# Performance work log

Hardware: AMD Instinct MI355X
Metric: run time of the kernel (lower is better)

Reference implementation:

```python
import jax, jax.numpy as jnp
import numpy as np

EPS = 1e-6      # VN nonlinearity eps
BN_EPS = 1e-5   # torch BatchNorm default eps


def setup_inputs() -> dict:
    key = jax.random.key(0)
    k1, k2, k3 = jax.random.split(key, 3)
    B, Cin, N = 8, 64, 2048
    Cout = 64
    x = jax.random.normal(k1, (B, Cin, 3, N), dtype=jnp.float32)
    # nn.Linear(in, out, bias=False) weights: [out, in], kaiming-uniform-ish scale
    s = 1.0 / np.sqrt(Cin)
    W_feat = jax.random.uniform(k2, (Cout, Cin), jnp.float32, -s, s)
    W_dir = jax.random.uniform(k3, (Cout, Cin), jnp.float32, -s, s)
    gamma = jnp.ones((Cout,), jnp.float32)
    beta = jnp.zeros((Cout,), jnp.float32)
    return {"x": x, "W_feat": W_feat, "W_dir": W_dir, "gamma": gamma, "beta": beta, "k": 10}


def _knn_idx(xf, kk):
    # xf: [B, D, N]; returns indices of kk nearest neighbors (incl. self), [B, N, kk]
    xx = jnp.sum(xf * xf, axis=1)                       # [B, N]
    inner = jnp.einsum('bdn,bdm->bnm', xf, xf)          # [B, N, N]
    pdist = 2.0 * inner - xx[:, :, None] - xx[:, None, :]  # = -||xi-xj||^2
    _, idx = jax.lax.top_k(pdist, kk)                   # largest = nearest
    return idx


def reference(x, W_feat, W_dir, gamma, beta, k):
    B, Cin, _, N = x.shape
    K = k + 1
    xf = x.reshape(B, Cin * 3, N)                       # [B, 3*Cin, N]
    idx = _knn_idx(xf, K)                               # [B, N, K]

    # gather neighbor features: [B, N, K, 3*Cin]
    xT = jnp.transpose(xf, (0, 2, 1))                   # [B, N, 3*Cin]
    feat = jax.vmap(lambda xt, id_: xt[id_])(xT, idx)   # [B, N, K, 3*Cin]
    feat = feat.reshape(B, N, K, Cin, 3)
    feat = jnp.transpose(feat, (0, 3, 4, 1, 2))         # [B, Cin, 3, N, K]

    # VN linear
    p = jnp.einsum('oc,bcdnk->bodnk', W_feat, feat)     # [B, Cout, 3, N, K]

    # VNBatchNorm (training-mode batch stats, biased var) on vector norms
    norm = jnp.sqrt(jnp.sum(p * p, axis=2))             # [B, Cout, N, K]
    mean = jnp.mean(norm, axis=(0, 2, 3))
    var = jnp.var(norm, axis=(0, 2, 3))
    norm_bn = (norm - mean[None, :, None, None]) * jax.lax.rsqrt(var + BN_EPS)[None, :, None, None]
    norm_bn = norm_bn * gamma[None, :, None, None] + beta[None, :, None, None]
    p = p / norm[:, :, None] * norm_bn[:, :, None]

    # direction + conditional vector nonlinearity
    d = jnp.einsum('oc,bcdnk->bodnk', W_dir, feat)      # [B, Cout, 3, N, K]
    dot = jnp.sum(p * d, axis=2, keepdims=True)         # [B, Cout, 1, N, K]
    d_sq = jnp.sum(d * d, axis=2, keepdims=True)
    x_out = jnp.where(dot >= 0, p, p - dot / (d_sq + EPS) * d)

    return jnp.mean(x_out, axis=-1)                     # [B, Cout, 3, N]
```

## Files before the change

kernel.cpp:

```cpp
#include <hip/hip_runtime.h>
#include <stdint.h>

#define B_   8
#define D_   192
#define N_   2048
#define KNb  11

using u32 = uint32_t;
using u16 = unsigned short;
typedef _Float16 f16;
struct alignas(8) h4 { f16 x, y, z, w; };

typedef __attribute__((ext_vector_type(8)))  short short8;
typedef __attribute__((ext_vector_type(16))) float f32x16;

__device__ __forceinline__ u16 f2bf(float f){
  union{float f; u32 i;} x; x.f = f;
  u32 r = (x.i + 0x7fffu + ((x.i >> 16) & 1u)) >> 16;
  return (u16)r;
}
__device__ __forceinline__ u32 umax32(u32 a, u32 b){ return a > b ? a : b; }
__device__ __forceinline__ u32 umin32(u32 a, u32 b){ return a < b ? a : b; }
__device__ __forceinline__ u32 med3_u32(u32 a, u32 b, u32 c){
  u32 d;
  asm("v_med3_u32 %0, %1, %2, %3" : "=v"(d) : "v"(a), "v"(b), "v"(c));
  return d;
}

__device__ __forceinline__ void sel16(const u32* __restrict__ ctp, u32* key){
  #pragma unroll
  for (int q = 0; q < 4; ++q){
    uint4 kv = *(const uint4*)(ctp + 4*q);
    u32 ks[4] = {kv.x, kv.y, kv.z, kv.w};
    #pragma unroll
    for (int j = 0; j < 4; ++j){
      u32 kk = ks[j];
      #pragma unroll
      for (int s = 0; s < 9; ++s) key[s] = med3_u32(kk, key[s], key[s+1]);
      key[9] = umax32(kk, key[9]);
    }
  }
}

__global__ __launch_bounds__(256) void split_kernel(const float* __restrict__ x,
                                                    short* __restrict__ Xs,
                                                    float* __restrict__ xT,
                                                    double* __restrict__ xxd){
  __shared__ float A[D_ * 32];
  const int b = blockIdx.y, tile = blockIdx.x, m0 = tile * 32, t = threadIdx.x;
  const size_t xb = (size_t)b * D_ * N_;
  #pragma unroll
  for (int q = 0; q < 24; ++q){
    int p = t + 256*q;
    int d = p >> 5, i = p & 31;
    A[d*32 + i] = x[xb + (size_t)d*N_ + m0 + i];
  }
  __syncthreads();

  {
    const int l = t & 63, wv = t >> 6;
    const int lh = l >> 5, l31 = l & 31;
    #pragma unroll
    for (int j = 0; j < 3; ++j){
      int c = j*4 + wv;
      int dbase = c*16 + lh*8;
      union{ u16 s[8]; int4 v; } u;
      #pragma unroll
      for (int q = 0; q < 8; ++q) u.s[q] = f2bf(A[(dbase + q)*32 + l31]);
      size_t P = ((size_t)b*64 + tile)*12 + c;
      *(int4*)(Xs + P*512 + l*8) = u.v;
    }
  }
  {
    const int m = t & 31, seg = t >> 5;
    float* trow = xT + ((size_t)b*N_ + m0 + m) * 192 + seg*24;
    #pragma unroll
    for (int j = 0; j < 6; ++j){
      float4 v = { A[(seg*24 + 4*j + 0)*32 + m], A[(seg*24 + 4*j + 1)*32 + m],
                   A[(seg*24 + 4*j + 2)*32 + m], A[(seg*24 + 4*j + 3)*32 + m] };
      *(float4*)(trow + 4*j) = v;
    }
  }
  if (t < 32){
    double s = 0.0;
    #pragma unroll 4
    for (int d = 0; d < D_; ++d){ double v = (double)A[d*32 + t]; s = fma(v, v, s); }
    xxd[b*N_ + m0 + t] = s;
  }
}

#define KLA   0
#define KLCT0 12288
#define KLCT1 45568
#define KLSZ  78848
__global__ __launch_bounds__(512, 4) void knn_kernel(const short* __restrict__ Xs,
                                                     const double* __restrict__ xxd,
                                                     u16* __restrict__ cand){
  __shared__ __align__(16) char smem[KLSZ];

  const int b = blockIdx.x, n0 = blockIdx.y * 32;
  const int t = threadIdx.x, lane = t & 63, w = t >> 6;
  const int l31 = lane & 31, lh = lane >> 5;
  const int mcol = w*32 + l31;

  {
    const short* Ap = Xs + (((size_t)b*64 + (n0 >> 5)) * 12) * 512;
    int4 v = *(const int4*)(Ap + (size_t)t*8);
    *(int4*)(smem + KLA + t*16) = v;
    if (t < 256){
      int p = t + 512;
      int4 v2 = *(const int4*)(Ap + (size_t)p*8);
      *(int4*)(smem + KLA + p*16) = v2;
    }
  }
  float xxn[16];
  #pragma unroll
  for (int reg = 0; reg < 16; ++reg){
    int r = (reg & 3) + 8*(reg >> 2) + 4*lh;
    xxn[reg] = (float)xxd[b*N_ + n0 + r];
  }
  __syncthreads();

  u32 key[10];
  #pragma unroll
  for (int j = 0; j < 10; ++j) key[j] = 0u;

  for (int st = 0; st < 8; ++st){
    const int m0 = st * 256;
    const short* Bp = Xs + (((size_t)b*64 + st*8 + w) * 12) * 512 + lane*8;
    short8 pg[12];
    #pragma unroll
    for (int j = 0; j < 12; ++j) pg[j] = *(const short8*)(Bp + j*512);
    float xxs = (float)xxd[b*N_ + m0 + mcol];

    if (st > 0){
      const u32* ctp = (const u32*)(smem + ((st & 1) ? KLCT0 : KLCT1))
                       + (t & 31)*260 + (t >> 5)*16;
      sel16(ctp, key);
    }

    f32x16 acc = (f32x16)0.0f;
    #pragma unroll
    for (int kc = 0; kc < 6; ++kc){
      short8 a0 = *(const short8*)(smem + KLA + (kc*2+0)*1024 + lane*16);
      short8 a1 = *(const short8*)(smem + KLA + (kc*2+1)*1024 + lane*16);
      acc = __builtin_amdgcn_mfma_f32_32x32x16_bf16(a0, pg[kc*2+0], acc, 0, 0, 0);
      acc = __builtin_amdgcn_mfma_f32_32x32x16_bf16(a1, pg[kc*2+1], acc, 0, 0, 0);
    }

    {
      u32* ctw = (u32*)(smem + ((st & 1) ? KLCT1 : KLCT0));
      const u32 midx = (u32)(m0 + mcol);
      #pragma unroll
      for (int reg = 0; reg < 16; ++reg){
        float v = fmaf(2.f, acc[reg], -(xxs + xxn[reg]));
        u32 bb = __float_as_uint(v);
        u32 kk = ((bb ^ (u32)(((int)bb >> 31) | 0x80000000)) & 0xFFFFF800u) | midx;
        int r = (reg & 3) + 8*(reg >> 2) + 4*lh;
        ctw[r*260 + mcol] = kk;
      }
    }
    __syncthreads();
  }
  {
    const u32* ctp = (const u32*)(smem + KLCT1) + (t & 31)*260 + (t >> 5)*16;
    sel16(ctp, key);
  }

  u32* MVK = (u32*)(smem + KLCT0);
  {
    const int r = t & 31, sub = t >> 5;
    #pragma unroll
    for (int j = 0; j < 10; ++j) MVK[(sub*32 + r)*10 + j] = key[j];
  }
  __syncthreads();
  if (t < 32){
    int head[16];
    #pragma unroll
    for (int q = 0; q < 16; ++q) head[q] = 9;
    const size_t ob = ((size_t)b*N_ + n0 + t) * 16;
    for (int s = 0; s < 16; ++s){
      u32 best = 0u; int bq = 0;
      #pragma unroll
      for (int q = 0; q < 16; ++q){
        int hh = head[q];
        u32 v = (hh >= 0) ? MVK[(q*32 + t)*10 + hh] : 0u;
        if (v > best){ best = v; bq = q; }
      }
      cand[ob + s] = (u16)(best & 2047u);
      #pragma unroll
      for (int q = 0; q < 16; ++q) head[q] -= (q == bq) ? 1 : 0;
    }
  }
}

__global__ __launch_bounds__(256, 3) void refine_kernel(const float* __restrict__ xT,
                                                        const u16* __restrict__ cand,
                                                        const double* __restrict__ xxd,
                                                        int* __restrict__ idxout,
                                                        int* __restrict__ cnt){
  const int wv = threadIdx.x >> 6, ln = threadIdx.x & 63;
  const int b = blockIdx.x & 7;
  const int n = (blockIdx.x >> 3) * 4 + wv;
  const int g = b * N_ + n;
  const int c = ln >> 2, part = ln & 3;
  const int m = (int)cand[(size_t)g*16 + c] & 2047;
  const float4* pn = (const float4*)(xT + ((size_t)b*N_ + n)*192 + part*48);
  const float4* pm = (const float4*)(xT + ((size_t)b*N_ + m)*192 + part*48);
  float4 an[12], am[12];
  #pragma unroll
  for (int j = 0; j < 12; ++j) an[j] = pn[j];
  #pragma unroll
  for (int j = 0; j < 12; ++j) am[j] = pm[j];
  double s0 = 0.0, s1 = 0.0, s2 = 0.0, s3 = 0.0;
  #pragma unroll
  for (int j = 0; j < 12; j += 4){
    s0 = fma((double)an[j+0].x, (double)am[j+0].x, s0);
    s0 = fma((double)an[j+0].y, (double)am[j+0].y, s0);
    s0 = fma((double)an[j+0].z, (double)am[j+0].z, s0);
    s0 = fma((double)an[j+0].w, (double)am[j+0].w, s0);
    s1 = fma((double)an[j+1].x, (double)am[j+1].x, s1);
    s1 = fma((double)an[j+1].y, (double)am[j+1].y, s1);
    s1 = fma((double)an[j+1].z, (double)am[j+1].z, s1);
    s1 = fma((double)an[j+1].w, (double)am[j+1].w, s1);
    s2 = fma((double)an[j+2].x, (double)am[j+2].x, s2);
    s2 = fma((double)an[j+2].y, (double)am[j+2].y, s2);
    s2 = fma((double)an[j+2].z, (double)am[j+2].z, s2);
    s2 = fma((double)an[j+2].w, (double)am[j+2].w, s2);
    s3 = fma((double)an[j+3].x, (double)am[j+3].x, s3);
    s3 = fma((double)an[j+3].y, (double)am[j+3].y, s3);
    s3 = fma((double)an[j+3].z, (double)am[j+3].z, s3);
    s3 = fma((double)an[j+3].w, (double)am[j+3].w, s3);
  }
  double s = (s0 + s1) + (s2 + s3);
  s += __shfl_down(s, 2, 64);
  s += __shfl_down(s, 1, 64);
  double v = 2.0*s - xxd[b*N_ + n] - xxd[b*N_ + m];
  int rank = 0;
  #pragma unroll
  for (int q = 0; q < 16; ++q){
    double vq = __shfl(v, q*4, 64);
    int    mq = __shfl(m, q*4, 64);
    bool beat = (vq > v) || ((vq == v) && (mq < m));
    rank += beat ? 1 : 0;
  }
  if (part == 0 && rank < KNb){
    idxout[(size_t)g*KNb + rank] = m;
    atomicAdd(&cnt[b*N_ + m], 1);
  }
}

__global__ __launch_bounds__(256) void project_kernel(const float* __restrict__ xT,
                                                      const float* __restrict__ Wf,
                                                      const float* __restrict__ Wd,
                                                      h4* __restrict__ P0h,
                                                      h4* __restrict__ D0h){
  __shared__ float A[16 * 192];
  const int b = blockIdx.x, m0 = blockIdx.y * 16, t = threadIdx.x;
  const int l = t & 63, wv = t >> 6;
  const int half = l >> 5;
  const int c = (wv & 1)*32 + (l & 31);
  const int mg = wv >> 1;

  float wfh[32], wdh[32];
  #pragma unroll
  for (int q = 0; q < 8; ++q){
    float4 uf = *(const float4*)(Wf + c*64 + half*32 + q*4);
    wfh[q*4+0]=uf.x; wfh[q*4+1]=uf.y; wfh[q*4+2]=uf.z; wfh[q*4+3]=uf.w;
    float4 ud = *(const float4*)(Wd + c*64 + half*32 + q*4);
    wdh[q*4+0]=ud.x; wdh[q*4+1]=ud.y; wdh[q*4+2]=ud.z; wdh[q*4+3]=ud.w;
  }
  {
    const float4* src = (const float4*)(xT + ((size_t)b*N_ + m0)*192);
    float4* dst = (float4*)A;
    #pragma unroll
    for (int j = 0; j < 3; ++j) dst[t + 256*j] = src[t + 256*j];
  }
  __syncthreads();

  for (int i = 0; i < 8; ++i){
    int m = mg*8 + i;
    const float4* row = (const float4*)(A + m*192 + half*96);
    float p[3] = {0.f,0.f,0.f}, qv[3] = {0.f,0.f,0.f};
    #pragma unroll
    for (int v4 = 0; v4 < 24; ++v4){
      float4 f = row[v4];
      const int e = v4*4;
      p [(e+0)%3] = fmaf(wfh[(e+0)/3], f.x, p [(e+0)%3]);
      qv[(e+0)%3] = fmaf(wdh[(e+0)/3], f.x, qv[(e+0)%3]);
      p [(e+1)%3] = fmaf(wfh[(e+1)/3], f.y, p [(e+1)%3]);
      qv[(e+1)%3] = fmaf(wdh[(e+1)/3], f.y, qv[(e+1)%3]);
      p [(e+2)%3] = fmaf(wfh[(e+2)/3], f.z, p [(e+2)%3]);
      qv[(e+2)%3] = fmaf(wdh[(e+2)/3], f.z, qv[(e+2)%3]);
      p [(e+3)%3] = fmaf(wfh[(e+3)/3], f.w, p [(e+3)%3]);
      qv[(e+3)%3] = fmaf(wdh[(e+3)/3], f.w, qv[(e+3)%3]);
    }
    float o0 = __shfl_xor(p[0], 32, 64), o1 = __shfl_xor(p[1], 32, 64);
    float o2 = __shfl_xor(p[2], 32, 64);
    float u0 = __shfl_xor(qv[0], 32, 64), u1 = __shfl_xor(qv[1], 32, 64);
    float u2 = __shfl_xor(qv[2], 32, 64);
    if (half == 0){
      float t0 = p[0] + o0, t1 = p[1] + o1, t2 = p[2] + o2;
      float r0 = qv[0] + u0, r1 = qv[1] + u1, r2 = qv[2] + u2;
      float nrm = sqrtf(t0*t0 + t1*t1 + t2*t2);
      float dsq = r0*r0 + r1*r1 + r2*r2;
      size_t base = ((size_t)b*N_ + m0 + m)*64 + c;
      h4 vp; vp.x = (f16)t0; vp.y = (f16)t1; vp.z = (f16)t2; vp.w = (f16)nrm;
      h4 vd; vd.x = (f16)r0; vd.y = (f16)r1; vd.z = (f16)r2; vd.w = (f16)dsq;
      P0h[base] = vp;
      D0h[base] = vd;
    }
  }
}

__global__ __launch_bounds__(256) void stats_kernel(const h4* __restrict__ P0h,
                                                    const int* __restrict__ cnt,
                                                    float* __restrict__ gs){
  const int b = blockIdx.x >> 6;
  const int chunk = blockIdx.x & 63;
  const int w = threadIdx.x >> 6, c = threadIdx.x & 63;
  float s = 0.f, s2 = 0.f;
  const int mbase = chunk*32 + w*8;
  for (int i = 0; i < 8; ++i){
    int m = mbase + i;
    float wt = (float)cnt[b*N_ + m];
    float nv = (float)P0h[((size_t)b*N_ + m)*64 + c].w;
    s  = fmaf(wt, nv, s);
    s2 = fmaf(wt*nv, nv, s2);
  }
  __shared__ float red[8][64];
  red[w][c] = s; red[4+w][c] = s2;
  __syncthreads();
  if (w == 0) atomicAdd(&gs[c],    red[0][c]+red[1][c]+red[2][c]+red[3][c]);
  if (w == 1) atomicAdd(&gs[64+c], red[4][c]+red[5][c]+red[6][c]+red[7][c]);
}

__global__ __launch_bounds__(512) void out_kernel(const h4* __restrict__ P0h, const h4* __restrict__ D0h,
                                                  const int* __restrict__ idxin, const float* __restrict__ gs,
                                                  const float* __restrict__ gamma, const float* __restrict__ beta,
                                                  float* __restrict__ outp){
  __shared__ float res[16 * 193];
  const int b  = blockIdx.x;
  const int n0 = blockIdx.y * 16;
  const int t = threadIdx.x, w = t >> 6, c = t & 63;
  const float Ninv = 1.f / (float)(B_*N_*KNb);
  float mean = gs[c] * Ninv;
  float var  = gs[64+c] * Ninv - mean*mean;
  float istd = rsqrtf(var + 1e-5f);
  float sa = istd * gamma[c];
  float be = beta[c];
  const float kinv = 1.f/11.f;
  for (int i = 0; i < 2; ++i){
    int row = w*2 + i;
    int n = n0 + row;
    const int* ip = idxin + ((size_t)b*N_ + n)*KNb;
    float a0=0, a1=0, a2=0;
    #pragma unroll
    for (int k = 0; k < KNb; ++k){
      int m = ip[k] & 2047;
      size_t base = ((size_t)b*N_ + m)*64 + c;
      h4 P  = P0h[base];
      h4 Dv = D0h[base];
      float pw = (float)P.w;
      float nb = (pw - mean)*sa + be;
      float sc = nb / pw;
      float p0 = (float)P.x*sc, p1 = (float)P.y*sc, p2 = (float)P.z*sc;
      float d0 = (float)Dv.x, d1 = (float)Dv.y, d2 = (float)Dv.z;
      float dot = p0*d0 + p1*d1 + p2*d2;
      float f = (dot >= 0.f) ? 0.f : dot / ((float)Dv.w + 1e-6f);
      a0 += p0 - f*d0; a1 += p1 - f*d1; a2 += p2 - f*d2;
    }
    res[row*193 + 3*c + 0] = a0*kinv;
    res[row*193 + 3*c + 1] = a1*kinv;
    res[row*193 + 3*c + 2] = a2*kinv;
  }
  __syncthreads();
  {
    int p = t;
    #pragma unroll
    for (int j = 0; j < 2; ++j){
      if (p < 768){
        int cdim = p >> 2, nq = p & 3;
        float4 v = { res[(nq*4 + 0)*193 + cdim], res[(nq*4 + 1)*193 + cdim],
                     res[(nq*4 + 2)*193 + cdim], res[(nq*4 + 3)*193 + cdim] };
        *(float4*)(outp + ((size_t)b*192 + cdim)*N_ + n0 + nq*4) = v;
      }
      p += 512;
    }
  }
}

extern "C" void kernel_launch(void* const* d_in, const int* in_sizes, int n_in,
                              void* d_out, int out_size, void* d_ws, size_t ws_size,
                              hipStream_t stream){
  const float* x     = (const float*)d_in[0];
  const float* Wf    = (const float*)d_in[1];
  const float* Wd    = (const float*)d_in[2];
  const float* gamma = (const float*)d_in[3];
  const float* beta  = (const float*)d_in[4];
  float* outp = (float*)d_out;

  char* ws = (char*)d_ws;
  int*    idx  = (int*)   (ws);
  int*    cnt  = (int*)   (ws + 720896);
  float*  gs   = (float*) (ws + 786432);
  h4*     P0h  = (h4*)    (ws + 1048576);
  h4*     D0h  = (h4*)    (ws + 9437184);
  short*  Xs   = (short*) (ws + 1048576);
  double* xxd  = (double*)(ws + 13631488);
  u16*    cand = (u16*)   (ws + 13762560);
  float*  xT   = (float*) (ws + 17825792);

  hipMemsetAsync(cnt, 0, 66048, stream);
  split_kernel  <<<dim3(64, 8),  256, 0, stream>>>(x, Xs, xT, xxd);
  knn_kernel    <<<dim3(8, 64),  512, 0, stream>>>(Xs, xxd, cand);
  refine_kernel <<<4096,         256, 0, stream>>>(xT, cand, xxd, idx, cnt);
  project_kernel<<<dim3(8, 128), 256, 0, stream>>>(xT, Wf, Wd, P0h, D0h);
  stats_kernel  <<<512,          256, 0, stream>>>(P0h, cnt, gs);
  out_kernel    <<<dim3(8, 128), 512, 0, stream>>>(P0h, D0h, idx, gs, gamma, beta, outp);
}
```

Measured before the change: 233.0 us.

## Skip idle top-k inserts and merge per-row candidates with wave shuffles

The top-k insertion network now runs only when some lane in the wave has a key larger than its current minimum. The 16 threads that own a query row are made contiguous (row = t>>4), so the final 16-way merge runs as a shuffle-based max reduction across 16 lanes. This replaces the shared-memory dump and the serial merge done by 32 threads. It removes a barrier and the single-warp tail, at the cost of a ballot branch inside the selection loop and a changed LDS access pattern for the candidate reads.

```diff
diff --git a/kernel.cpp b/kernel.cpp
--- a/kernel.cpp
+++ b/kernel.cpp
@@ -35,9 +35,11 @@
     #pragma unroll
     for (int j = 0; j < 4; ++j){
       u32 kk = ks[j];
-      #pragma unroll
-      for (int s = 0; s < 9; ++s) key[s] = med3_u32(kk, key[s], key[s+1]);
-      key[9] = umax32(kk, key[9]);
+      if (__any(kk > key[0])){
+        #pragma unroll
+        for (int s = 0; s < 9; ++s) key[s] = med3_u32(kk, key[s], key[s+1]);
+        key[9] = umax32(kk, key[9]);
+      }
     }
   }
 }
@@ -102,6 +104,7 @@
   const int t = threadIdx.x, lane = t & 63, w = t >> 6;
   const int l31 = lane & 31, lh = lane >> 5;
   const int mcol = w*32 + l31;
+  const int selr = t >> 4, selg = t & 15;
 
   {
     const short* Ap = Xs + (((size_t)b*64 + (n0 >> 5)) * 12) * 512;
@@ -135,7 +138,7 @@
 
     if (st > 0){
       const u32* ctp = (const u32*)(smem + ((st & 1) ? KLCT0 : KLCT1))
-                       + (t & 31)*260 + (t >> 5)*16;
+                       + selr*260 + selg*16;
       sel16(ctp, key);
     }
 
@@ -163,34 +166,25 @@
     __syncthreads();
   }
   {
-    const u32* ctp = (const u32*)(smem + KLCT1) + (t & 31)*260 + (t >> 5)*16;
+    const u32* ctp = (const u32*)(smem + KLCT1) + selr*260 + selg*16;
     sel16(ctp, key);
   }
 
-  u32* MVK = (u32*)(smem + KLCT0);
-  {
-    const int r = t & 31, sub = t >> 5;
-    #pragma unroll
-    for (int j = 0; j < 10; ++j) MVK[(sub*32 + r)*10 + j] = key[j];
-  }
-  __syncthreads();
-  if (t < 32){
-    int head[16];
-    #pragma unroll
-    for (int q = 0; q < 16; ++q) head[q] = 9;
-    const size_t ob = ((size_t)b*N_ + n0 + t) * 16;
+  {
+    u32 mycand = 0u;
+    #pragma unroll
     for (int s = 0; s < 16; ++s){
-      u32 best = 0u; int bq = 0;
+      u32 h = key[9];
+      u32 wm = h;
       #pragma unroll
-      for (int q = 0; q < 16; ++q){
-        int hh = head[q];
-        u32 v = (hh >= 0) ? MVK[(q*32 + t)*10 + hh] : 0u;
-        if (v > best){ best = v; bq = q; }
-      }
-      cand[ob + s] = (u16)(best & 2047u);
+      for (int d = 1; d < 16; d <<= 1) wm = umax32(wm, __shfl_xor(wm, d, 16));
+      bool win = (h == wm);
       #pragma unroll
-      for (int q = 0; q < 16; ++q) head[q] -= (q == bq) ? 1 : 0;
-    }
+      for (int q = 9; q > 0; --q) key[q] = win ? key[q-1] : key[q];
+      key[0] = win ? 0u : key[0];
+      mycand = (selg == s) ? wm : mycand;
+    }
+    cand[((size_t)b*N_ + n0 + selr)*16 + selg] = (u16)(mycand & 2047u);
   }
 }
 
```

Result: no change. 228.8 us (-1.8%).
